# Kernel optimization log

Hardware: AMD Instinct MI355X
Metric: run time of the kernel (lower is better)

## Reference

```python
import jax, jax.numpy as jnp
import numpy as np

N_NODES = 50000
N_EDGES = 800000
NUM_FEAT = 256
HID = 64
N_CLS = 40
N_LAYERS = 2
EPS = 0.3  # residual scale from __init__ eps


def setup_inputs() -> dict:
    key = jax.random.key(0)
    ks = jax.random.split(key, 8)
    x = jax.random.normal(ks[0], (N_NODES, NUM_FEAT), dtype=jnp.float32)
    edge_index = jax.random.randint(ks[1], (2, N_EDGES), 0, N_NODES, dtype=jnp.int64)
    # xavier-normal-ish scaled weights
    W1 = jax.random.normal(ks[2], (HID, NUM_FEAT), dtype=jnp.float32) * (1.414 * (2.0 / (HID + NUM_FEAT)) ** 0.5)
    b1 = jnp.zeros((HID,), dtype=jnp.float32)
    W2 = jax.random.normal(ks[3], (N_CLS, HID), dtype=jnp.float32) * (1.414 * (2.0 / (N_CLS + HID)) ** 0.5)
    b2 = jnp.zeros((N_CLS,), dtype=jnp.float32)
    gate_w = jax.random.normal(ks[4], (N_LAYERS, 2 * HID), dtype=jnp.float32) * (1.414 * (2.0 / (2 * HID + 1)) ** 0.5)
    gate_b = jnp.zeros((N_LAYERS,), dtype=jnp.float32)
    return {"x": x, "edge_index": edge_index, "W1": W1, "b1": b1,
            "W2": W2, "b2": b2, "gate_w": gate_w, "gate_b": gate_b}


def _forward(x, edge_index, W1, b1, W2, b2, gate_w, gate_b):
    row, col = edge_index[0], edge_index[1]  # row = source, col = target (PyG convention)
    n = x.shape[0]
    ones_e = jnp.ones((edge_index.shape[1],), dtype=x.dtype)
    # degree(row) clamped to >=1, then d^{-1/2}
    deg = jnp.clip(jax.ops.segment_sum(ones_e, row, num_segments=n), 1.0)
    nd = deg ** -0.5  # [N]
    # mean-aggregation denominator: incoming-edge counts per target node
    cnt = jnp.clip(jax.ops.segment_sum(ones_e, col, num_segments=n), 1.0)

    # dense input projection (dropout is eval-mode no-op)
    h = jax.nn.relu(x @ W1.T + b1)  # [N, H]
    raw = h

    nd_edge = nd[row] * nd[col]  # [E]
    for l in range(N_LAYERS):
        hr = h[row]  # [E, H] gather (source)
        hc = h[col]  # [E, H] gather (target)
        # gate: Linear(concat([h[row], h[col]])) == h[row]@w_a + h[col]@w_b
        g = jnp.tanh(hr @ gate_w[l, :HID] + hc @ gate_w[l, HID:] + gate_b[l])  # [E]
        norm = g * nd_edge  # [E]
        msg = norm[:, None] * (hc + hr)  # x_i + x_j, [E, H]
        agg = jax.ops.segment_sum(msg, col, num_segments=n) / cnt[:, None]  # scatter-mean
        h = EPS * raw + agg

    logits = h @ W2.T + b2
    return jax.nn.log_softmax(logits, axis=1)


def reference(x, edge_index, W1, b1, W2, b2, gate_w, gate_b):
    return _forward(x, edge_index, W1, b1, W2, b2, gate_w, gate_b)
```

## Files before the change

### kernel.cpp

```cpp
#include <hip/hip_runtime.h>
#include <math.h>

#define N_NODES 50000
#define N_EDGES 800000
#define NFEAT 256
#define HID 64
#define NCLS 40
#define EPS_RES 0.3f
#define SCAN_BLOCKS ((N_NODES + 255) / 256)
#define EB 32
#define CHUNK (N_EDGES / EB)
#define NR 4
#define RNG (N_NODES / NR)

typedef unsigned int uint;
typedef unsigned short ushort;
typedef __attribute__((ext_vector_type(8))) short short8v;
typedef __attribute__((ext_vector_type(4))) float f32x4;

__device__ __forceinline__ float bflo(uint u) { return __uint_as_float(u << 16); }
__device__ __forceinline__ float bfhi(uint u) { return __uint_as_float(u & 0xFFFF0000u); }
__device__ __forceinline__ uint bf16rne(float f) {
    uint u = __float_as_uint(f);
    return (u + 0x7FFFu + ((u >> 16) & 1u)) >> 16;
}
__device__ __forceinline__ uint bf16rne2(float a, float b) {
    return bf16rne(a) | (bf16rne(b) << 16);
}

__device__ __forceinline__ void bfsplit(float v, ushort& h, ushort& l) {
    uint hb_ = bf16rne(v);
    float hf = __uint_as_float(hb_ << 16);
    uint lb_ = bf16rne(v - hf);
    h = (ushort)hb_;
    l = (ushort)lb_;
}

__device__ __forceinline__ float fast_tanh(float x) {
    float t = __builtin_amdgcn_exp2f(x * 2.885390081777927f);
    return 1.0f - 2.0f * __builtin_amdgcn_rcpf(t + 1.0f);
}

__global__ __launch_bounds__(256) void hist_kernel(const int* __restrict__ row,
                                                   const int* __restrict__ col,
                                                   int* __restrict__ degM,
                                                   int* __restrict__ cntM,
                                                   int* __restrict__ rank_local) {
    __shared__ int hist[RNG];
    int t = threadIdx.x;
    int chunk = blockIdx.x;
    int lo = blockIdx.y * RNG;
    int side = blockIdx.z;
    for (int j = t; j < RNG; j += 256) hist[j] = 0;
    __syncthreads();
    const int* idx = side ? col : row;
    int e0 = chunk * CHUNK;
    if (side == 0) {
        for (int base = 0; base < CHUNK; base += 1024) {
            int vb[4];
#pragma unroll
            for (int j = 0; j < 4; j++) {
                int i = base + j * 256 + t;
                vb[j] = (i < CHUNK) ? idx[e0 + i] : -1;
            }
#pragma unroll
            for (int j = 0; j < 4; j++) {
                uint v = (uint)(vb[j] - lo);
                if (v < RNG) atomicAdd(&hist[v], 1);
            }
        }
    } else {
        for (int base = 0; base < CHUNK; base += 1024) {
            int vb[4], ib[4];
#pragma unroll
            for (int j = 0; j < 4; j++) {
                int i = base + j * 256 + t;
                ib[j] = i;
                vb[j] = (i < CHUNK) ? idx[e0 + i] : -1;
            }
#pragma unroll
            for (int j = 0; j < 4; j++) {
                uint v = (uint)(vb[j] - lo);
                if (v < RNG) rank_local[e0 + ib[j]] = atomicAdd(&hist[v], 1);
            }
        }
    }
    __syncthreads();
    int* M = side ? cntM : degM;
    for (int j = t; j < RNG; j += 256) M[chunk * N_NODES + lo + j] = hist[j];
}

__device__ __forceinline__ int block_excl_scan_256(int v, int t, int* wsum) {
    int lane = t & 63, w = t >> 6;
    int sv = v;
#pragma unroll
    for (int d = 1; d < 64; d <<= 1) {
        int o = __shfl_up(sv, d);
        if (lane >= d) sv += o;
    }
    if (lane == 63) wsum[w] = sv;
    __syncthreads();
    int add = 0;
    for (int i = 0; i < w; i++) add += wsum[i];
    return sv + add - v;
}

__global__ void scan1_kernel(const int* __restrict__ degM, int* __restrict__ cntM,
                             int* __restrict__ off, int* __restrict__ bsum,
                             float* __restrict__ nd, float* __restrict__ invcnt) {
    __shared__ int wsum[4];
    int t = threadIdx.x;
    int idx = blockIdx.x * 256 + t;
    int v = 0;
    if (idx < N_NODES) {
        int sD = 0;
#pragma unroll
        for (int c = 0; c < EB; c++) sD += degM[c * N_NODES + idx];
        int run = 0;
#pragma unroll
        for (int c = 0; c < EB; c++) {
            int cv = cntM[c * N_NODES + idx];
            cntM[c * N_NODES + idx] = run;
            run += cv;
        }
        v = run;
        if (sD < 1) sD = 1;
        nd[idx] = rsqrtf((float)sD);
        int cc = run; if (cc < 1) cc = 1;
        invcnt[idx] = 1.0f / (float)cc;
    }
    int excl = block_excl_scan_256(v, t, wsum);
    if (idx < N_NODES) off[idx] = excl;
    if (t == 255) bsum[blockIdx.x] = excl + v;
}

__global__ void scan2_kernel(int* __restrict__ bsum) {
    __shared__ int wsum[4];
    int t = threadIdx.x;
    int v = (t < SCAN_BLOCKS) ? bsum[t] : 0;
    int excl = block_excl_scan_256(v, t, wsum);
    if (t < SCAN_BLOCKS) bsum[t] = excl;
}

__global__ void scan3_kernel(int* __restrict__ off, const int* __restrict__ bsum) {
    int t = threadIdx.x;
    int idx = blockIdx.x * 256 + t;
    if (idx < N_NODES) off[idx] += bsum[blockIdx.x];
    if (idx == 0) off[N_NODES] = N_EDGES;
}

__global__ void scatter_kernel(const int* __restrict__ row, const int* __restrict__ col,
                               const int* __restrict__ rank_local, const int* __restrict__ cntM,
                               const int* __restrict__ off, const float* __restrict__ nd,
                               int2* __restrict__ sedge) {
    int e = blockIdx.x * 256 + threadIdx.x;
    int r = row[e], c = col[e];
    int ch = e / CHUNK;
    int p = off[c] + cntM[ch * N_NODES + c] + rank_local[e];
    int2 se;
    se.x = r;
    se.y = __float_as_int(nd[r] * nd[c]);
    sedge[p] = se;
}

__global__ __launch_bounds__(256) void proj_kernel(const float* __restrict__ x,
                                                   const float* __restrict__ W1,
                                                   const float* __restrict__ b1,
                                                   const float* __restrict__ gw,
                                                   float* __restrict__ ha,
                                                   ushort* __restrict__ habf,
                                                   float* __restrict__ y,
                                                   float* __restrict__ z) {
    __shared__ ushort smem[4 * 64 * 72];
    ushort* xs_h = smem;
    ushort* xs_l = smem + 4608;
    ushort* ws_h = smem + 9216;
    ushort* ws_l = smem + 13824;
    int t = threadIdx.x;
    int nb = blockIdx.x * 64;
    int lane = t & 63, w = t >> 6;
    int l15 = lane & 15, g = lane >> 4;
    int hbase = 16 * w + 4 * g;

    f32x4 acc[4];
#pragma unroll
    for (int hb = 0; hb < 4; hb++) acc[hb] = (f32x4)0.f;

    for (int kc = 0; kc < NFEAT; kc += 64) {
        __syncthreads();
#pragma unroll
        for (int i = 0; i < 4; i++) {
            int idx = t + 256 * i;
            int r_ = idx >> 4;
            int kq = idx & 15;
            int gn = nb + r_;
            float4 v = make_float4(0.f, 0.f, 0.f, 0.f);
            if (gn < N_NODES) v = *(const float4*)(x + (size_t)gn * NFEAT + kc + kq * 4);
            ushort4 h4, l4;
            bfsplit(v.x, h4.x, l4.x);
            bfsplit(v.y, h4.y, l4.y);
            bfsplit(v.z, h4.z, l4.z);
            bfsplit(v.w, h4.w, l4.w);
            *(ushort4*)(xs_h + r_ * 72 + kq * 4) = h4;
            *(ushort4*)(xs_l + r_ * 72 + kq * 4) = l4;
            float4 wv = *(const float4*)(W1 + (size_t)r_ * NFEAT + kc + kq * 4);
            bfsplit(wv.x, h4.x, l4.x);
            bfsplit(wv.y, h4.y, l4.y);
            bfsplit(wv.z, h4.z, l4.z);
            bfsplit(wv.w, h4.w, l4.w);
            *(ushort4*)(ws_h + r_ * 72 + kq * 4) = h4;
            *(ushort4*)(ws_l + r_ * 72 + kq * 4) = l4;
        }
        __syncthreads();
#pragma unroll
        for (int ko = 0; ko < 2; ko++) {
            int koff = ko * 32 + g * 8;
            short8v a_h = *(const short8v*)(xs_h + (w * 16 + l15) * 72 + koff);
            short8v a_l = *(const short8v*)(xs_l + (w * 16 + l15) * 72 + koff);
            short8v b_h[4], b_l[4];
#pragma unroll
            for (int hb = 0; hb < 4; hb++) {
                b_h[hb] = *(const short8v*)(ws_h + (hb * 16 + l15) * 72 + koff);
                b_l[hb] = *(const short8v*)(ws_l + (hb * 16 + l15) * 72 + koff);
            }
#pragma unroll
            for (int hb = 0; hb < 4; hb++) {
                acc[hb] = __builtin_amdgcn_mfma_f32_16x16x32_bf16(a_h, b_h[hb], acc[hb], 0, 0, 0);
                acc[hb] = __builtin_amdgcn_mfma_f32_16x16x32_bf16(a_h, b_l[hb], acc[hb], 0, 0, 0);
                acc[hb] = __builtin_amdgcn_mfma_f32_16x16x32_bf16(a_l, b_h[hb], acc[hb], 0, 0, 0);
            }
        }
    }
    __syncthreads();
    float* hsf = (float*)smem;
    float* ypart = hsf + 64 * 68;
    float* zpart = ypart + 1024;
#pragma unroll
    for (int hb = 0; hb < 4; hb++)
#pragma unroll
        for (int r = 0; r < 4; r++) {
            int nl = w * 16 + g * 4 + r;
            hsf[nl * 68 + hb * 16 + l15] = acc[hb][r];
        }
    __syncthreads();
    float4 bias = *(const float4*)(b1 + hbase);
    float4 wa4 = *(const float4*)(gw + hbase);
    float4 wb4 = *(const float4*)(gw + HID + hbase);
    int slot = w * 4 + g;
#pragma unroll
    for (int j = 0; j < 4; j++) {
        int rowl = l15 + 16 * j;
        int gn = nb + rowl;
        float4 hv = *(const float4*)(hsf + rowl * 68 + hbase);
        float4 o;
        o.x = fmaxf(hv.x + bias.x, 0.f);
        o.y = fmaxf(hv.y + bias.y, 0.f);
        o.z = fmaxf(hv.z + bias.z, 0.f);
        o.w = fmaxf(hv.w + bias.w, 0.f);
        if (gn < N_NODES) {
            *(float4*)(ha + (size_t)gn * HID + hbase) = o;
            uint2 pk;
            pk.x = bf16rne2(o.x, o.y);
            pk.y = bf16rne2(o.z, o.w);
            *(uint2*)(habf + (size_t)gn * HID + hbase) = pk;
        }
        ypart[rowl * 16 + slot] = o.x * wa4.x + o.y * wa4.y + o.z * wa4.z + o.w * wa4.w;
        zpart[rowl * 16 + slot] = o.x * wb4.x + o.y * wb4.y + o.z * wb4.z + o.w * wb4.w;
    }
    __syncthreads();
    if (t < 64 && nb + t < N_NODES) {
        float sa = 0.f, sb = 0.f;
#pragma unroll
        for (int s = 0; s < 16; s++) { sa += ypart[t * 16 + s]; sb += zpart[t * 16 + s]; }
        y[nb + t] = sa;
        z[nb + t] = sb;
    }
}

__device__ __forceinline__ void agg_group8(const ushort* __restrict__ hbf,
                                           const int2* __restrict__ sedge,
                                           const float* __restrict__ yv,
                                           float zc, int e0, int d, int c8,
                                           float acc[8], float& gs_out) {
    float accE[8], accO[8];
#pragma unroll
    for (int i = 0; i < 8; i++) { accE[i] = 0.f; accO[i] = 0.f; }
    float gsE = 0.f, gsO = 0.f;
    int m = d;
    m = max(m, __shfl_xor(m, 8));
    m = max(m, __shfl_xor(m, 16));
    m = max(m, __shfl_xor(m, 32));
    int mp = (m + 1) >> 1;
    if (mp > 0) {
#define LOADSE(p, seE, seO, ndeE, ndeO)                                         \
        {   int k2_ = 2 * (p);                                                  \
            seE = sedge[(k2_ < d) ? e0 + k2_ : 0];                              \
            ndeE = (k2_ < d) ? __int_as_float(seE.y) : 0.f;                     \
            seO = sedge[(k2_ + 1 < d) ? e0 + k2_ + 1 : 0];                      \
            ndeO = (k2_ + 1 < d) ? __int_as_float(seO.y) : 0.f; }
#define LOADUY(seE, seO, yE, yO, uE, uO)                                        \
        {   yE = yv[seE.x];                                                     \
            uE = *(const uint4*)(hbf + (size_t)seE.x * HID + c8);               \
            yO = yv[seO.x];                                                     \
            uO = *(const uint4*)(hbf + (size_t)seO.x * HID + c8); }
        int2 seEA, seOA, seEB, seOB, seEC, seOC;
        float ndeEA, ndeOA, ndeEB, ndeOB, ndeEC, ndeOC;
        float yEA, yOA, yEB, yOB;
        uint4 uEA, uOA, uEB, uOB;
        LOADSE(0, seEA, seOA, ndeEA, ndeOA);
        LOADSE(1, seEB, seOB, ndeEB, ndeOB);
        LOADSE(2, seEC, seOC, ndeEC, ndeOC);
        LOADUY(seEA, seOA, yEA, yOA, uEA, uOA);
        LOADUY(seEB, seOB, yEB, yOB, uEB, uOB);
        for (int p = 0; p < mp; ++p) {
            float yEC, yOC; uint4 uEC, uOC;
            LOADUY(seEC, seOC, yEC, yOC, uEC, uOC);
            int2 seED, seOD; float ndeED, ndeOD;
            LOADSE(p + 3, seED, seOD, ndeED, ndeOD);
            float gvE = fast_tanh(yEA + zc) * ndeEA;
            accE[0] += gvE * bflo(uEA.x);
            accE[1] += gvE * bfhi(uEA.x);
            accE[2] += gvE * bflo(uEA.y);
            accE[3] += gvE * bfhi(uEA.y);
            accE[4] += gvE * bflo(uEA.z);
            accE[5] += gvE * bfhi(uEA.z);
            accE[6] += gvE * bflo(uEA.w);
            accE[7] += gvE * bfhi(uEA.w);
            gsE += gvE;
            float gvO = fast_tanh(yOA + zc) * ndeOA;
            accO[0] += gvO * bflo(uOA.x);
            accO[1] += gvO * bfhi(uOA.x);
            accO[2] += gvO * bflo(uOA.y);
            accO[3] += gvO * bfhi(uOA.y);
            accO[4] += gvO * bflo(uOA.z);
            accO[5] += gvO * bfhi(uOA.z);
            accO[6] += gvO * bflo(uOA.w);
            accO[7] += gvO * bfhi(uOA.w);
            gsO += gvO;
            yEA = yEB; uEA = uEB; ndeEA = ndeEB;
            yOA = yOB; uOA = uOB; ndeOA = ndeOB;
            yEB = yEC; uEB = uEC; ndeEB = ndeEC;
            yOB = yOC; uOB = uOC; ndeOB = ndeOC;
            seEC = seED; seOC = seOD; ndeEC = ndeED; ndeOC = ndeOD;
        }
#undef LOADSE
#undef LOADUY
    }
#pragma unroll
    for (int i = 0; i < 8; i++) acc[i] = accE[i] + accO[i];
    gs_out = gsE + gsO;
}

__global__ __launch_bounds__(256) void agg1_kernel(
        const float* __restrict__ ha, const ushort* __restrict__ habf,
        const int2* __restrict__ sedge, const int* __restrict__ off,
        const float* __restrict__ invcnt, const float* __restrict__ y,
        const float* __restrict__ z, const float* __restrict__ gb,
        const float* __restrict__ gw2, ushort* __restrict__ hbbf,
        float* __restrict__ y2, float* __restrict__ z2) {
    int t = threadIdx.x;
    int lane = t & 63;
    int ln = t >> 3;
    int node = blockIdx.x * 32 + ln;
    int nc = (node < N_NODES) ? node : (N_NODES - 1);
    int c8 = (lane & 7) * 8;
    int e0 = off[nc];
    int e1 = off[nc + 1];
    int d = (node < N_NODES) ? (e1 - e0) : 0;
    float zc = z[nc] + gb[0];
    float acc[8]; float gs;
    agg_group8(habf, sedge, y, zc, e0, d, c8, acc, gs);
    float invc = invcnt[nc];
    float4 ra = *(const float4*)(ha + (size_t)nc * HID + c8);
    float4 rb = *(const float4*)(ha + (size_t)nc * HID + c8 + 4);
    float raw8[8] = {ra.x, ra.y, ra.z, ra.w, rb.x, rb.y, rb.z, rb.w};
    float o[8];
#pragma unroll
    for (int i = 0; i < 8; i++) o[i] = EPS_RES * raw8[i] + (acc[i] + gs * raw8[i]) * invc;
    if (node < N_NODES) {
        uint4 pk;
        pk.x = bf16rne2(o[0], o[1]);
        pk.y = bf16rne2(o[2], o[3]);
        pk.z = bf16rne2(o[4], o[5]);
        pk.w = bf16rne2(o[6], o[7]);
        *(uint4*)(hbbf + (size_t)nc * HID + c8) = pk;
    }
    float4 wa0 = *(const float4*)(gw2 + c8);
    float4 wa1 = *(const float4*)(gw2 + c8 + 4);
    float4 wb0 = *(const float4*)(gw2 + HID + c8);
    float4 wb1 = *(const float4*)(gw2 + HID + c8 + 4);
    float p = o[0] * wa0.x + o[1] * wa0.y + o[2] * wa0.z + o[3] * wa0.w
            + o[4] * wa1.x + o[5] * wa1.y + o[6] * wa1.z + o[7] * wa1.w;
    float qq = o[0] * wb0.x + o[1] * wb0.y + o[2] * wb0.z + o[3] * wb0.w
             + o[4] * wb1.x + o[5] * wb1.y + o[6] * wb1.z + o[7] * wb1.w;
#pragma unroll
    for (int s = 1; s < 8; s <<= 1) { p += __shfl_xor(p, s); qq += __shfl_xor(qq, s); }
    if ((lane & 7) == 0 && node < N_NODES) { y2[node] = p; z2[node] = qq; }
}

__global__ __launch_bounds__(256) void agg2_kernel(
        const ushort* __restrict__ hbbf, const float* __restrict__ ha,
        const int2* __restrict__ sedge, const int* __restrict__ off,
        const float* __restrict__ invcnt, const float* __restrict__ y2,
        const float* __restrict__ z2, const float* __restrict__ gb,
        const float* __restrict__ W2, const float* __restrict__ b2,
        float* __restrict__ out) {
    __shared__ float w2s[NCLS * 72];
    __shared__ float b2s[NCLS];
    __shared__ float hs[32 * 72];
    int t = threadIdx.x;
    for (int i = t; i < NCLS * HID; i += 256) w2s[(i >> 6) * 72 + (i & 63)] = W2[i];
    if (t < NCLS) b2s[t] = b2[t];
    int lane = t & 63;
    int ln = t >> 3;
    int node = blockIdx.x * 32 + ln;
    int nc = (node < N_NODES) ? node : (N_NODES - 1);
    int c8 = (lane & 7) * 8;
    int e0 = off[nc];
    int e1 = off[nc + 1];
    int d = (node < N_NODES) ? (e1 - e0) : 0;
    float zc = z2[nc] + gb[0];
    float acc[8]; float gs;
    agg_group8(hbbf, sedge, y2, zc, e0, d, c8, acc, gs);
    float invc = invcnt[nc];
    uint4 hc = *(const uint4*)(hbbf + (size_t)nc * HID + c8);
    float hcv[8] = {bflo(hc.x), bfhi(hc.x), bflo(hc.y), bfhi(hc.y),
                    bflo(hc.z), bfhi(hc.z), bflo(hc.w), bfhi(hc.w)};
    float4 ra = *(const float4*)(ha + (size_t)nc * HID + c8);
    float4 rb = *(const float4*)(ha + (size_t)nc * HID + c8 + 4);
    float raw8[8] = {ra.x, ra.y, ra.z, ra.w, rb.x, rb.y, rb.z, rb.w};
    float4 o0, o1;
    o0.x = EPS_RES * raw8[0] + (acc[0] + gs * hcv[0]) * invc;
    o0.y = EPS_RES * raw8[1] + (acc[1] + gs * hcv[1]) * invc;
    o0.z = EPS_RES * raw8[2] + (acc[2] + gs * hcv[2]) * invc;
    o0.w = EPS_RES * raw8[3] + (acc[3] + gs * hcv[3]) * invc;
    o1.x = EPS_RES * raw8[4] + (acc[4] + gs * hcv[4]) * invc;
    o1.y = EPS_RES * raw8[5] + (acc[5] + gs * hcv[5]) * invc;
    o1.z = EPS_RES * raw8[6] + (acc[6] + gs * hcv[6]) * invc;
    o1.w = EPS_RES * raw8[7] + (acc[7] + gs * hcv[7]) * invc;
    *(float4*)(hs + ln * 72 + c8) = o0;
    *(float4*)(hs + ln * 72 + c8 + 4) = o1;
    __syncthreads();
    int k5 = t & 7;
    float lg[5];
#pragma unroll
    for (int j = 0; j < 5; j++) lg[j] = b2s[k5 + 8 * j];
    const float* hrow = hs + ln * 72;
#pragma unroll
    for (int j4 = 0; j4 < 16; j4++) {
        float4 h4 = *(const float4*)(hrow + j4 * 4);
#pragma unroll
        for (int j = 0; j < 5; j++) {
            float4 w4 = *(const float4*)(w2s + (k5 + 8 * j) * 72 + j4 * 4);
            lg[j] += h4.x * w4.x + h4.y * w4.y + h4.z * w4.z + h4.w * w4.w;
        }
    }
    float v = fmaxf(fmaxf(fmaxf(lg[0], lg[1]), fmaxf(lg[2], lg[3])), lg[4]);
    v = fmaxf(v, __shfl_xor(v, 1));
    v = fmaxf(v, __shfl_xor(v, 2));
    v = fmaxf(v, __shfl_xor(v, 4));
    float ex = 0.f;
#pragma unroll
    for (int j = 0; j < 5; j++) ex += __builtin_amdgcn_exp2f((lg[j] - v) * 1.44269504088896f);
    ex += __shfl_xor(ex, 1);
    ex += __shfl_xor(ex, 2);
    ex += __shfl_xor(ex, 4);
    float ls = v + __builtin_amdgcn_logf(ex) * 0.693147180559945f;
    if (node < N_NODES) {
#pragma unroll
        for (int j = 0; j < 5; j++) out[(size_t)node * NCLS + k5 + 8 * j] = lg[j] - ls;
    }
}

extern "C" void kernel_launch(void* const* d_in, const int* in_sizes, int n_in,
                              void* d_out, int out_size, void* d_ws, size_t ws_size,
                              hipStream_t stream) {
    const float* x  = (const float*)d_in[0];
    const int*   ei = (const int*)d_in[1];
    const float* W1 = (const float*)d_in[2];
    const float* b1 = (const float*)d_in[3];
    const float* W2 = (const float*)d_in[4];
    const float* b2 = (const float*)d_in[5];
    const float* gw = (const float*)d_in[6];
    const float* gb = (const float*)d_in[7];
    float* out = (float*)d_out;

    int2*  sedge  = (int2*)d_ws;
    float* nd     = (float*)(sedge + N_EDGES);
    float* invcnt = nd + N_NODES;
    float* y      = invcnt + N_NODES;
    float* z      = y + N_NODES;
    float* y2     = z + N_NODES;
    float* z2     = y2 + N_NODES;
    float* ha     = z2 + N_NODES;
    ushort* habf  = (ushort*)(ha + (size_t)N_NODES * HID);
    ushort* hbbf  = habf + (size_t)N_NODES * HID;
    int*   off    = (int*)(hbbf + (size_t)N_NODES * HID);
    int*   bsum   = off + N_NODES + 1;
    int*   degM   = (int*)ha;
    int*   cntM   = degM + (size_t)EB * N_NODES;
    int*   rank_local = (int*)habf;

    const int* row = ei;
    const int* col = ei + N_EDGES;

    hist_kernel<<<dim3(EB, NR, 2), 256, 0, stream>>>(row, col, degM, cntM, rank_local);
    scan1_kernel<<<SCAN_BLOCKS, 256, 0, stream>>>(degM, cntM, off, bsum, nd, invcnt);
    scan2_kernel<<<1, 256, 0, stream>>>(bsum);
    scan3_kernel<<<SCAN_BLOCKS, 256, 0, stream>>>(off, bsum);
    scatter_kernel<<<N_EDGES / 256, 256, 0, stream>>>(row, col, rank_local, cntM, off, nd, sedge);
    proj_kernel<<<(N_NODES + 63) / 64, 256, 0, stream>>>(x, W1, b1, gw, ha, habf, y, z);

    int aggblocks = (N_NODES + 31) / 32;
    agg1_kernel<<<aggblocks, 256, 0, stream>>>(ha, habf, sedge, off, invcnt, y, z, gb,
                                               gw + 2 * HID, hbbf, y2, z2);
    agg2_kernel<<<aggblocks, 256, 0, stream>>>(hbbf, ha, sedge, off, invcnt, y2, z2,
                                               gb + 1, W2, b2, out);
}
```

Baseline: 217.5 us.

## Sort nodes by in-degree via counting sort to balance aggregation work

Builds a degree histogram with 1024 bins in the scan kernels and produces a permutation of nodes grouped by in-degree. Both aggregation kernels then process nodes in that order, so the 8 node groups in a wavefront have similar edge counts and less time is lost to divergence. In exchange, the scan phase gains global atomics, the permutation adds an indirect load and makes node writes non-contiguous, and nodes within a bin land in nondeterministic order.

```diff
diff --git a/kernel.cpp b/kernel.cpp
--- a/kernel.cpp
+++ b/kernel.cpp
@@ -12,6 +12,7 @@
 #define CHUNK (N_EDGES / EB)
 #define NR 4
 #define RNG (N_NODES / NR)
+#define DBINS 1024
 
 typedef unsigned int uint;
 typedef unsigned short ushort;
@@ -45,12 +46,16 @@
                                                    const int* __restrict__ col,
                                                    int* __restrict__ degM,
                                                    int* __restrict__ cntM,
-                                                   int* __restrict__ rank_local) {
+                                                   int* __restrict__ rank_local,
+                                                   int* __restrict__ binCnt) {
     __shared__ int hist[RNG];
     int t = threadIdx.x;
     int chunk = blockIdx.x;
     int lo = blockIdx.y * RNG;
     int side = blockIdx.z;
+    if (chunk == 0 && blockIdx.y == 0 && side == 0) {
+        for (int j = t; j < DBINS; j += 256) binCnt[j] = 0;
+    }
     for (int j = t; j < RNG; j += 256) hist[j] = 0;
     __syncthreads();
     const int* idx = side ? col : row;
@@ -107,7 +112,8 @@
 
 __global__ void scan1_kernel(const int* __restrict__ degM, int* __restrict__ cntM,
                              int* __restrict__ off, int* __restrict__ bsum,
-                             float* __restrict__ nd, float* __restrict__ invcnt) {
+                             float* __restrict__ nd, float* __restrict__ invcnt,
+                             int* __restrict__ binCnt, int* __restrict__ degv) {
     __shared__ int wsum[4];
     int t = threadIdx.x;
     int idx = blockIdx.x * 256 + t;
@@ -128,24 +134,49 @@
         nd[idx] = rsqrtf((float)sD);
         int cc = run; if (cc < 1) cc = 1;
         invcnt[idx] = 1.0f / (float)cc;
+        int db = (run < DBINS) ? run : (DBINS - 1);
+        degv[idx] = db;
+        atomicAdd(&binCnt[db], 1);
     }
     int excl = block_excl_scan_256(v, t, wsum);
     if (idx < N_NODES) off[idx] = excl;
     if (t == 255) bsum[blockIdx.x] = excl + v;
 }
 
-__global__ void scan2_kernel(int* __restrict__ bsum) {
+__global__ void scan2_kernel(int* __restrict__ bsum, const int* __restrict__ binCnt,
+                             int* __restrict__ binBase, int* __restrict__ binCursor) {
     __shared__ int wsum[4];
+    __shared__ int wsum2[4];
     int t = threadIdx.x;
     int v = (t < SCAN_BLOCKS) ? bsum[t] : 0;
     int excl = block_excl_scan_256(v, t, wsum);
     if (t < SCAN_BLOCKS) bsum[t] = excl;
-}
-
-__global__ void scan3_kernel(int* __restrict__ off, const int* __restrict__ bsum) {
+    int b4[4];
+    int s = 0;
+#pragma unroll
+    for (int i = 0; i < 4; i++) { b4[i] = binCnt[t * 4 + i]; s += b4[i]; }
+    __syncthreads();
+    int base = block_excl_scan_256(s, t, wsum2);
+    int rsum = base;
+#pragma unroll
+    for (int i = 0; i < 4; i++) {
+        binBase[t * 4 + i] = rsum;
+        binCursor[t * 4 + i] = 0;
+        rsum += b4[i];
+    }
+}
+
+__global__ void scan3_kernel(int* __restrict__ off, const int* __restrict__ bsum,
+                             const int* __restrict__ degv, const int* __restrict__ binBase,
+                             int* __restrict__ binCursor, int* __restrict__ perm) {
     int t = threadIdx.x;
     int idx = blockIdx.x * 256 + t;
-    if (idx < N_NODES) off[idx] += bsum[blockIdx.x];
+    if (idx < N_NODES) {
+        off[idx] += bsum[blockIdx.x];
+        int d = degv[idx];
+        int pos = binBase[d] + atomicAdd(&binCursor[d], 1);
+        perm[pos] = idx;
+    }
     if (idx == 0) off[N_NODES] = N_EDGES;
 }
 
@@ -356,12 +387,13 @@
         const int2* __restrict__ sedge, const int* __restrict__ off,
         const float* __restrict__ invcnt, const float* __restrict__ y,
         const float* __restrict__ z, const float* __restrict__ gb,
-        const float* __restrict__ gw2, ushort* __restrict__ hbbf,
-        float* __restrict__ y2, float* __restrict__ z2) {
+        const float* __restrict__ gw2, const int* __restrict__ perm,
+        ushort* __restrict__ hbbf, float* __restrict__ y2, float* __restrict__ z2) {
     int t = threadIdx.x;
     int lane = t & 63;
     int ln = t >> 3;
-    int node = blockIdx.x * 32 + ln;
+    int pidx = blockIdx.x * 32 + ln;
+    int node = (pidx < N_NODES) ? perm[pidx] : N_NODES;
     int nc = (node < N_NODES) ? node : (N_NODES - 1);
     int c8 = (lane & 7) * 8;
     int e0 = off[nc];
@@ -404,7 +436,7 @@
         const float* __restrict__ invcnt, const float* __restrict__ y2,
         const float* __restrict__ z2, const float* __restrict__ gb,
         const float* __restrict__ W2, const float* __restrict__ b2,
-        float* __restrict__ out) {
+        const int* __restrict__ perm, float* __restrict__ out) {
     __shared__ float w2s[NCLS * 72];
     __shared__ float b2s[NCLS];
     __shared__ float hs[32 * 72];
@@ -413,7 +445,8 @@
     if (t < NCLS) b2s[t] = b2[t];
     int lane = t & 63;
     int ln = t >> 3;
-    int node = blockIdx.x * 32 + ln;
+    int pidx = blockIdx.x * 32 + ln;
+    int node = (pidx < N_NODES) ? perm[pidx] : N_NODES;
     int nc = (node < N_NODES) ? node : (N_NODES - 1);
     int c8 = (lane & 7) * 8;
     int e0 = off[nc];
@@ -497,6 +530,11 @@
     ushort* hbbf  = habf + (size_t)N_NODES * HID;
     int*   off    = (int*)(hbbf + (size_t)N_NODES * HID);
     int*   bsum   = off + N_NODES + 1;
+    int*   binCnt = bsum + 256;
+    int*   binBase = binCnt + DBINS;
+    int*   binCursor = binBase + DBINS;
+    int*   degv   = binCursor + DBINS;
+    int*   perm   = degv + N_NODES;
     int*   degM   = (int*)ha;
     int*   cntM   = degM + (size_t)EB * N_NODES;
     int*   rank_local = (int*)habf;
@@ -504,16 +542,17 @@
     const int* row = ei;
     const int* col = ei + N_EDGES;
 
-    hist_kernel<<<dim3(EB, NR, 2), 256, 0, stream>>>(row, col, degM, cntM, rank_local);
-    scan1_kernel<<<SCAN_BLOCKS, 256, 0, stream>>>(degM, cntM, off, bsum, nd, invcnt);
-    scan2_kernel<<<1, 256, 0, stream>>>(bsum);
-    scan3_kernel<<<SCAN_BLOCKS, 256, 0, stream>>>(off, bsum);
+    hist_kernel<<<dim3(EB, NR, 2), 256, 0, stream>>>(row, col, degM, cntM, rank_local, binCnt);
+    scan1_kernel<<<SCAN_BLOCKS, 256, 0, stream>>>(degM, cntM, off, bsum, nd, invcnt,
+                                                  binCnt, degv);
+    scan2_kernel<<<1, 256, 0, stream>>>(bsum, binCnt, binBase, binCursor);
+    scan3_kernel<<<SCAN_BLOCKS, 256, 0, stream>>>(off, bsum, degv, binBase, binCursor, perm);
     scatter_kernel<<<N_EDGES / 256, 256, 0, stream>>>(row, col, rank_local, cntM, off, nd, sedge);
     proj_kernel<<<(N_NODES + 63) / 64, 256, 0, stream>>>(x, W1, b1, gw, ha, habf, y, z);
 
     int aggblocks = (N_NODES + 31) / 32;
     agg1_kernel<<<aggblocks, 256, 0, stream>>>(ha, habf, sedge, off, invcnt, y, z, gb,
-                                               gw + 2 * HID, hbbf, y2, z2);
+                                               gw + 2 * HID, perm, hbbf, y2, z2);
     agg2_kernel<<<aggblocks, 256, 0, stream>>>(hbbf, ha, sedge, off, invcnt, y2, z2,
-                                               gb + 1, W2, b2, out);
-}
+                                               gb + 1, W2, b2, perm, out);
+}
```

Measured after the change: 459.9 us. +111.4%, slower.

## Sort nodes by in-degree bucket to balance aggregation wavefronts

Applied to the files above, without the earlier changes.

Adds a counting sort of nodes by incoming-edge count (capped at 64 bins) inside the existing scan kernels, producing a permutation. The two aggregation kernels then process nodes in permuted order, so the 8-lane groups within a wavefront have similar degrees and waste fewer idle cycles on divergent edge loops. The cost is extra scan work, a perm array, and loss of locality in node-indexed reads and writes (ha, off, outputs become scattered).

```diff
diff --git a/kernel.cpp b/kernel.cpp
--- a/kernel.cpp
+++ b/kernel.cpp
@@ -12,6 +12,7 @@
 #define CHUNK (N_EDGES / EB)
 #define NR 4
 #define RNG (N_NODES / NR)
+#define DBINS 64
 
 typedef unsigned int uint;
 typedef unsigned short ushort;
@@ -107,9 +108,13 @@
 
 __global__ void scan1_kernel(const int* __restrict__ degM, int* __restrict__ cntM,
                              int* __restrict__ off, int* __restrict__ bsum,
-                             float* __restrict__ nd, float* __restrict__ invcnt) {
+                             float* __restrict__ nd, float* __restrict__ invcnt,
+                             int* __restrict__ binCntM, int* __restrict__ degv) {
     __shared__ int wsum[4];
-    int t = threadIdx.x;
+    __shared__ int dhist[DBINS];
+    int t = threadIdx.x;
+    if (t < DBINS) dhist[t] = 0;
+    __syncthreads();
     int idx = blockIdx.x * 256 + t;
     int v = 0;
     if (idx < N_NODES) {
@@ -128,24 +133,56 @@
         nd[idx] = rsqrtf((float)sD);
         int cc = run; if (cc < 1) cc = 1;
         invcnt[idx] = 1.0f / (float)cc;
-    }
+        int db = (run < DBINS) ? run : (DBINS - 1);
+        int lrank = atomicAdd(&dhist[db], 1);
+        degv[idx] = db | (lrank << 6);
+    }
+    __syncthreads();
+    if (t < DBINS) binCntM[blockIdx.x * DBINS + t] = dhist[t];
     int excl = block_excl_scan_256(v, t, wsum);
     if (idx < N_NODES) off[idx] = excl;
     if (t == 255) bsum[blockIdx.x] = excl + v;
 }
 
-__global__ void scan2_kernel(int* __restrict__ bsum) {
+__global__ void scan2_kernel(int* __restrict__ bsum, int* __restrict__ binCntM) {
     __shared__ int wsum[4];
     int t = threadIdx.x;
     int v = (t < SCAN_BLOCKS) ? bsum[t] : 0;
     int excl = block_excl_scan_256(v, t, wsum);
     if (t < SCAN_BLOCKS) bsum[t] = excl;
-}
-
-__global__ void scan3_kernel(int* __restrict__ off, const int* __restrict__ bsum) {
+    __syncthreads();
+    if (t < DBINS) {
+        int tot = 0;
+#pragma unroll 4
+        for (int b = 0; b < SCAN_BLOCKS; b++) tot += binCntM[b * DBINS + t];
+        int sv = tot;
+#pragma unroll
+        for (int d2 = 1; d2 < 64; d2 <<= 1) {
+            int o = __shfl_up(sv, d2);
+            if (t >= d2) sv += o;
+        }
+        int run = sv - tot;
+#pragma unroll 4
+        for (int b = 0; b < SCAN_BLOCKS; b++) {
+            int c = binCntM[b * DBINS + t];
+            binCntM[b * DBINS + t] = run;
+            run += c;
+        }
+    }
+}
+
+__global__ void scan3_kernel(int* __restrict__ off, const int* __restrict__ bsum,
+                             const int* __restrict__ degv, const int* __restrict__ binCntM,
+                             int* __restrict__ perm) {
     int t = threadIdx.x;
     int idx = blockIdx.x * 256 + t;
-    if (idx < N_NODES) off[idx] += bsum[blockIdx.x];
+    if (idx < N_NODES) {
+        off[idx] += bsum[blockIdx.x];
+        int dv = degv[idx];
+        int db = dv & (DBINS - 1);
+        int lrank = dv >> 6;
+        perm[binCntM[blockIdx.x * DBINS + db] + lrank] = idx;
+    }
     if (idx == 0) off[N_NODES] = N_EDGES;
 }
 
@@ -356,12 +393,13 @@
         const int2* __restrict__ sedge, const int* __restrict__ off,
         const float* __restrict__ invcnt, const float* __restrict__ y,
         const float* __restrict__ z, const float* __restrict__ gb,
-        const float* __restrict__ gw2, ushort* __restrict__ hbbf,
-        float* __restrict__ y2, float* __restrict__ z2) {
+        const float* __restrict__ gw2, const int* __restrict__ perm,
+        ushort* __restrict__ hbbf, float* __restrict__ y2, float* __restrict__ z2) {
     int t = threadIdx.x;
     int lane = t & 63;
     int ln = t >> 3;
-    int node = blockIdx.x * 32 + ln;
+    int pidx = blockIdx.x * 32 + ln;
+    int node = (pidx < N_NODES) ? perm[pidx] : N_NODES;
     int nc = (node < N_NODES) ? node : (N_NODES - 1);
     int c8 = (lane & 7) * 8;
     int e0 = off[nc];
@@ -404,7 +442,7 @@
         const float* __restrict__ invcnt, const float* __restrict__ y2,
         const float* __restrict__ z2, const float* __restrict__ gb,
         const float* __restrict__ W2, const float* __restrict__ b2,
-        float* __restrict__ out) {
+        const int* __restrict__ perm, float* __restrict__ out) {
     __shared__ float w2s[NCLS * 72];
     __shared__ float b2s[NCLS];
     __shared__ float hs[32 * 72];
@@ -413,7 +451,8 @@
     if (t < NCLS) b2s[t] = b2[t];
     int lane = t & 63;
     int ln = t >> 3;
-    int node = blockIdx.x * 32 + ln;
+    int pidx = blockIdx.x * 32 + ln;
+    int node = (pidx < N_NODES) ? perm[pidx] : N_NODES;
     int nc = (node < N_NODES) ? node : (N_NODES - 1);
     int c8 = (lane & 7) * 8;
     int e0 = off[nc];
@@ -497,6 +536,9 @@
     ushort* hbbf  = habf + (size_t)N_NODES * HID;
     int*   off    = (int*)(hbbf + (size_t)N_NODES * HID);
     int*   bsum   = off + N_NODES + 1;
+    int*   binCntM = bsum + 256;
+    int*   degv   = binCntM + SCAN_BLOCKS * DBINS;
+    int*   perm   = degv + N_NODES;
     int*   degM   = (int*)ha;
     int*   cntM   = degM + (size_t)EB * N_NODES;
     int*   rank_local = (int*)habf;
@@ -505,15 +547,16 @@
     const int* col = ei + N_EDGES;
 
     hist_kernel<<<dim3(EB, NR, 2), 256, 0, stream>>>(row, col, degM, cntM, rank_local);
-    scan1_kernel<<<SCAN_BLOCKS, 256, 0, stream>>>(degM, cntM, off, bsum, nd, invcnt);
-    scan2_kernel<<<1, 256, 0, stream>>>(bsum);
-    scan3_kernel<<<SCAN_BLOCKS, 256, 0, stream>>>(off, bsum);
+    scan1_kernel<<<SCAN_BLOCKS, 256, 0, stream>>>(degM, cntM, off, bsum, nd, invcnt,
+                                                  binCntM, degv);
+    scan2_kernel<<<1, 256, 0, stream>>>(bsum, binCntM);
+    scan3_kernel<<<SCAN_BLOCKS, 256, 0, stream>>>(off, bsum, degv, binCntM, perm);
     scatter_kernel<<<N_EDGES / 256, 256, 0, stream>>>(row, col, rank_local, cntM, off, nd, sedge);
     proj_kernel<<<(N_NODES + 63) / 64, 256, 0, stream>>>(x, W1, b1, gw, ha, habf, y, z);
 
     int aggblocks = (N_NODES + 31) / 32;
     agg1_kernel<<<aggblocks, 256, 0, stream>>>(ha, habf, sedge, off, invcnt, y, z, gb,
-                                               gw + 2 * HID, hbbf, y2, z2);
+                                               gw + 2 * HID, perm, hbbf, y2, z2);
     agg2_kernel<<<aggblocks, 256, 0, stream>>>(hbbf, ha, sedge, off, invcnt, y2, z2,
-                                               gb + 1, W2, b2, out);
-}
+                                               gb + 1, W2, b2, perm, out);
+}
```

After: 240.3 us. 10.5% more time.
